# Kernel tuning notes

Hardware: AMD Instinct MI355X
Metric: run time of the kernel (lower is better)

The kernel has to match this reference:

```python
import jax, jax.numpy as jnp
import numpy as np

B_SZ = 1
SEQ = 4096
IN_DIM = 1024
D_MODEL = 512
D_INNER = 1024   # expand(2) * d_model
D_STATE = 16
D_CONV = 4
DT_RANK = 32     # ceil(d_model / 16)
N_LAYERS = 2
N_CLASSES = 2


def setup_inputs() -> dict:
    key = jax.random.key(0)
    ks = jax.random.split(key, 12)
    s = 0.02
    x = jax.random.normal(ks[0], (B_SZ, SEQ, IN_DIM), jnp.float32)
    fc1_w = jax.random.normal(ks[1], (D_MODEL, IN_DIM), jnp.float32) * s
    fc1_b = jnp.zeros((D_MODEL,), jnp.float32)
    ln_w = jnp.ones((N_LAYERS, D_MODEL), jnp.float32)
    ln_b = jnp.zeros((N_LAYERS, D_MODEL), jnp.float32)
    in_proj_w = jax.random.normal(ks[2], (N_LAYERS, 2 * D_INNER, D_MODEL), jnp.float32) * s
    conv_w = jax.random.normal(ks[3], (N_LAYERS, D_INNER, D_CONV), jnp.float32) * 0.1
    conv_b = jnp.zeros((N_LAYERS, D_INNER), jnp.float32)
    x_proj_w = jax.random.normal(ks[4], (N_LAYERS, DT_RANK + 2 * D_STATE, D_INNER), jnp.float32) * s
    dt_proj_w = jax.random.normal(ks[5], (N_LAYERS, D_INNER, DT_RANK), jnp.float32) * s
    # bias so softplus(bias) ~ 0.01 (typical dt init)
    dt_proj_b = jnp.full((N_LAYERS, D_INNER), float(np.log(np.expm1(0.01))), jnp.float32)
    A_log = jnp.broadcast_to(jnp.log(jnp.arange(1, D_STATE + 1, dtype=jnp.float32)),
                             (N_LAYERS, D_INNER, D_STATE)).copy()
    D_skip = jnp.ones((N_LAYERS, D_INNER), jnp.float32)
    norm_w = jnp.ones((D_MODEL,), jnp.float32)
    norm_b = jnp.zeros((D_MODEL,), jnp.float32)
    cls_w = jax.random.normal(ks[6], (N_CLASSES, D_MODEL), jnp.float32) * s
    cls_b = jnp.zeros((N_CLASSES,), jnp.float32)
    return {"x": x, "fc1_w": fc1_w, "fc1_b": fc1_b, "ln_w": ln_w, "ln_b": ln_b,
            "in_proj_w": in_proj_w, "conv_w": conv_w, "conv_b": conv_b,
            "x_proj_w": x_proj_w, "dt_proj_w": dt_proj_w, "dt_proj_b": dt_proj_b,
            "A_log": A_log, "D_skip": D_skip, "norm_w": norm_w, "norm_b": norm_b,
            "cls_w": cls_w, "cls_b": cls_b}


def layernorm(h, w, b, eps=1e-5):
    mu = h.mean(-1, keepdims=True)
    var = ((h - mu) ** 2).mean(-1, keepdims=True)
    return (h - mu) * jax.lax.rsqrt(var + eps) * w + b


def mamba_block(h, in_proj_w, conv_w, conv_b, x_proj_w, dt_proj_w, dt_proj_b, A_log, D_skip):
    # h: [B, L, d_model]
    xz = jnp.einsum('bld,ed->ble', h, in_proj_w)          # [B, L, 2*D_INNER]
    xc, z = jnp.split(xz, 2, axis=-1)                     # each [B, L, D_INNER]
    # causal depthwise conv along L (kernel D_CONV)
    xp = jnp.pad(xc, ((0, 0), (D_CONV - 1, 0), (0, 0)))
    conv = sum(xp[:, k:k + xc.shape[1], :] * conv_w[:, k] for k in range(D_CONV))
    xc = jax.nn.silu(conv + conv_b)
    dbc = jnp.einsum('bld,ed->ble', xc, x_proj_w)         # [B, L, DT_RANK + 2*N]
    dt = jax.nn.softplus(jnp.einsum('blr,dr->bld', dbc[..., :DT_RANK], dt_proj_w) + dt_proj_b)
    Bm = dbc[..., DT_RANK:DT_RANK + D_STATE]              # [B, L, N]
    Cm = dbc[..., DT_RANK + D_STATE:]                     # [B, L, N]
    A = -jnp.exp(A_log)                                   # [D_INNER, N]
    dA = jnp.exp(dt[..., None] * A)                       # [B, L, D_INNER, N]
    dBx = dt[..., None] * Bm[:, :, None, :] * xc[..., None]

    def step(s, ins):
        dA_t, dBx_t, C_t = ins
        s = dA_t * s + dBx_t                              # [B, D_INNER, N]
        y = jnp.einsum('bdn,bn->bd', s, C_t)
        return s, y

    s0 = jnp.zeros((h.shape[0], D_INNER, D_STATE), h.dtype)
    _, ys = jax.lax.scan(step, s0, (dA.transpose(1, 0, 2, 3),
                                    dBx.transpose(1, 0, 2, 3),
                                    Cm.transpose(1, 0, 2)))
    y = ys.transpose(1, 0, 2) + xc * D_skip               # [B, L, D_INNER]
    y = y * jax.nn.silu(z)
    return y


def reference(x, fc1_w, fc1_b, ln_w, ln_b, in_proj_w, conv_w, conv_b,
              x_proj_w, dt_proj_w, dt_proj_b, A_log, D_skip,
              norm_w, norm_b, cls_w, cls_b):
    # out_proj of each Mamba layer folded: out_proj_w stored in in_proj? No -> build here.
    # We use the last N_LAYERS rows trick not needed: out projection is d_inner->d_model,
    # reuse in_proj_w transposed halves would be unfaithful, so derive deterministic weights.
    out_proj_w = jnp.stack([
        jax.random.normal(jax.random.fold_in(jax.random.key(7), i),
                          (D_MODEL, D_INNER), jnp.float32) * 0.02
        for i in range(N_LAYERS)])
    h = jax.nn.gelu(jnp.einsum('bli,di->bld', x, fc1_w) + fc1_b)
    for i in range(N_LAYERS):
        res = h
        hn = layernorm(h, ln_w[i], ln_b[i])
        y = mamba_block(hn, in_proj_w[i], conv_w[i], conv_b[i], x_proj_w[i],
                        dt_proj_w[i], dt_proj_b[i], A_log[i], D_skip[i])
        h = jnp.einsum('ble,de->bld', y, out_proj_w[i]) + res
    h = layernorm(h, norm_w, norm_b)
    hidden = h.mean(axis=1)                               # avg aggregation
    pred = hidden @ cls_w.T + cls_b
    return hidden, pred, h
```

## Files before the change

kernel.cpp:

```cpp
#include <hip/hip_runtime.h>
#include <cstdint>
#include <cstddef>

#define SEQ     4096
#define IN_DIM  1024
#define D_MODEL 512
#define D_INNER 1024
#define D_STATE 16
#define DT_RANK 32

#define CHUNK   32
#define NCHUNK  128
#define NREC    16384

#define LOG2E 1.44269504088896f

static const size_t OFF_H     = 0;
static const size_t OFF_PS    = 2097152;
static const size_t OFF_Z     = 6291456;
static const size_t OFF_XC    = 10485760;
static const size_t OFF_DT    = 14680064;
static const size_t OFF_CARRY = 18874368;
static const size_t OFF_HNB   = 20971520;
static const size_t OFF_WIB   = 21495808;
static const size_t OFF_DBCF  = 22020096;
static const size_t OFF_DBCB  = 22282240;
static const size_t OFF_XPWB  = 22413312;
static const size_t OFF_DPWB  = 22446080;
static const size_t OFF_WOUTB = 22462464;
static const size_t OFF_PART  = 22986752;

typedef __attribute__((ext_vector_type(8))) short bf16x8;
typedef __attribute__((ext_vector_type(4))) float f32x4;

__device__ __forceinline__ uint32_t rotl32(uint32_t v, int r) { return (v << r) | (v >> (32 - r)); }

__device__ __forceinline__ void threefry2x32(uint32_t k0, uint32_t k1, uint32_t x0, uint32_t x1,
                                             uint32_t& o0, uint32_t& o1) {
  uint32_t ks0 = k0, ks1 = k1, ks2 = k0 ^ k1 ^ 0x1BD11BDAu;
  x0 += ks0; x1 += ks1;
  const int rotA[4] = {13, 15, 26, 6};
  const int rotB[4] = {17, 29, 16, 24};
  uint32_t ks[3] = {ks0, ks1, ks2};
#pragma unroll
  for (int r = 0; r < 5; ++r) {
    const int* rr = (r & 1) ? rotB : rotA;
#pragma unroll
    for (int j = 0; j < 4; ++j) { x0 += x1; x1 = rotl32(x1, rr[j]); x1 ^= x0; }
    x0 += ks[(r + 1) % 3];
    x1 += ks[(r + 2) % 3] + (uint32_t)(r + 1);
  }
  o0 = x0; o1 = x1;
}

__device__ __forceinline__ float erfinv32(float x) {
  float w = -log1pf(-x * x);
  float p;
  if (w < 5.0f) {
    w -= 2.5f;
    p = 2.81022636e-08f;
    p = fmaf(p, w, 3.43273939e-07f);
    p = fmaf(p, w, -3.5233877e-06f);
    p = fmaf(p, w, -4.39150654e-06f);
    p = fmaf(p, w, 0.00021858087f);
    p = fmaf(p, w, -0.00125372503f);
    p = fmaf(p, w, -0.00417768164f);
    p = fmaf(p, w, 0.246640727f);
    p = fmaf(p, w, 1.50140941f);
  } else {
    w = sqrtf(w) - 3.0f;
    p = -0.000200214257f;
    p = fmaf(p, w, 0.000100950558f);
    p = fmaf(p, w, 0.00134934322f);
    p = fmaf(p, w, -0.00367342844f);
    p = fmaf(p, w, 0.00573950773f);
    p = fmaf(p, w, -0.0076224613f);
    p = fmaf(p, w, 0.00943887047f);
    p = fmaf(p, w, 1.00167406f);
    p = fmaf(p, w, 2.83297682f);
  }
  return p * x;
}

__device__ __forceinline__ float bits_to_normal(uint32_t b) {
  float f = __uint_as_float((b >> 9) | 0x3f800000u) - 1.0f;
  const float lo = -0.99999994f;
  float u = f * (1.0f - lo) + lo;
  u = fmaxf(lo, u);
  return 1.41421356f * erfinv32(u);
}

__device__ __forceinline__ ushort f2bf(float x) {
  uint32_t u = __float_as_uint(x);
  u = (u + 0x7FFFu + ((u >> 16) & 1u)) >> 16;
  return (ushort)u;
}
__device__ __forceinline__ bf16x8 pack8(float4 a, float4 b) {
  bf16x8 v;
  v[0] = f2bf(a.x); v[1] = f2bf(a.y); v[2] = f2bf(a.z); v[3] = f2bf(a.w);
  v[4] = f2bf(b.x); v[5] = f2bf(b.y); v[6] = f2bf(b.z); v[7] = f2bf(b.w);
  return v;
}

__global__ __launch_bounds__(256) void gen_wout(ushort* __restrict__ w) {
  int gid = blockIdx.x * 256 + threadIdx.x;
  int layer = gid >> 19;
  int j = gid & 0x7FFFF;
  uint32_t k0, k1;
  threefry2x32(0u, 7u, 0u, (uint32_t)layer, k0, k1);
  uint32_t o0, o1;
  threefry2x32(k0, k1, 0u, (uint32_t)j, o0, o1);
  w[(size_t)layer * 524288 + j] = f2bf(bits_to_normal(o0 ^ o1) * 0.02f);
}

__global__ __launch_bounds__(256) void f32_to_bf16(const float* __restrict__ in,
                                                   ushort* __restrict__ out, int n8) {
  int i = blockIdx.x * 256 + threadIdx.x;
  if (i >= n8) return;
  const float4* p = (const float4*)(in + (size_t)i * 8);
  *(bf16x8*)(out + (size_t)i * 8) = pack8(p[0], p[1]);
}

__device__ __forceinline__ float silu_f(float v) { return v / (1.0f + exp2f(-LOG2E * v)); }
__device__ __forceinline__ float gelu_f(float v) {
  float v3 = v * v * v;
  return 0.5f * v * (1.0f + tanhf(0.7978845608028654f * (v + 0.044715f * v3)));
}
__device__ __forceinline__ float softplus_f(float v) {
  return fmaxf(v, 0.0f) + log1pf(exp2f(-LOG2E * fabsf(v)));
}

enum { EPI_NONE = 0, EPI_BIAS_GELU = 1, EPI_INPROJ = 2, EPI_SOFTPLUS = 3, EPI_RESID = 4, EPI_DBC = 5 };

template <int EPI, int NT>
__global__ __launch_bounds__(256) void gemm_bf(
    const ushort* __restrict__ A, int lda,
    const ushort* __restrict__ B, int ldb,
    float* __restrict__ C, int ldc, int K,
    const float* __restrict__ bias, float* __restrict__ out2,
    ushort* __restrict__ outb) {
  constexpr int NB = NT / 64;
  __shared__ ushort As[2][64][40];
  __shared__ ushort Bs[2][NT][40];
  const int m0 = blockIdx.y * 64, n0 = blockIdx.x * NT;
  const int tid = threadIdx.x;
  const int arow = tid >> 2, ach = (tid & 3) * 8;
  const int lane = tid & 63, wid = tid >> 6;
  const int lr = lane & 15, lhi = lane >> 4;
  const ushort* Ap  = A + (size_t)(m0 + arow) * lda + ach;
  const ushort* Bp0 = B + (size_t)(n0 + arow) * ldb + ach;
  const ushort* Bp1 = (NB > 1) ? (B + (size_t)(n0 + 64 + arow) * ldb + ach) : Bp0;

  f32x4 acc[NT / 16] = {};
  uint4 ra, rb0, rb1;

  ra  = *(const uint4*)Ap;
  rb0 = *(const uint4*)Bp0;
  if (NB > 1) rb1 = *(const uint4*)Bp1;
  *(uint4*)&As[0][arow][ach] = ra;
  *(uint4*)&Bs[0][arow][ach] = rb0;
  if (NB > 1) *(uint4*)&Bs[0][64 + arow][ach] = rb1;
  __syncthreads();

  const int nk = K >> 5;
  int cur = 0;
  for (int ki = 0; ki < nk; ++ki) {
    const bool more = (ki + 1 < nk);
    if (more) {
      const int k = (ki + 1) << 5;
      ra  = *(const uint4*)(Ap + k);
      rb0 = *(const uint4*)(Bp0 + k);
      if (NB > 1) rb1 = *(const uint4*)(Bp1 + k);
    }
    bf16x8 af = *(const bf16x8*)&As[cur][wid * 16 + lr][lhi * 8];
#pragma unroll
    for (int t = 0; t < NT / 16; ++t) {
      bf16x8 bv = *(const bf16x8*)&Bs[cur][t * 16 + lr][lhi * 8];
      acc[t] = __builtin_amdgcn_mfma_f32_16x16x32_bf16(af, bv, acc[t], 0, 0, 0);
    }
    if (more) {
      *(uint4*)&As[cur ^ 1][arow][ach] = ra;
      *(uint4*)&Bs[cur ^ 1][arow][ach] = rb0;
      if (NB > 1) *(uint4*)&Bs[cur ^ 1][64 + arow][ach] = rb1;
    }
    __syncthreads();
    cur ^= 1;
  }

#pragma unroll
  for (int t = 0; t < NT / 16; ++t) {
    const int n = n0 + t * 16 + lr;
#pragma unroll
    for (int r = 0; r < 4; ++r) {
      const int m = m0 + wid * 16 + lhi * 4 + r;
      float v = acc[t][r];
      if (EPI == EPI_NONE) {
        C[(size_t)m * ldc + n] = v;
      } else if (EPI == EPI_BIAS_GELU) {
        v += bias[n];
        C[(size_t)m * ldc + n] = gelu_f(v);
      } else if (EPI == EPI_SOFTPLUS) {
        v += bias[n];
        C[(size_t)m * ldc + n] = softplus_f(v);
      } else if (EPI == EPI_RESID) {
        C[(size_t)m * ldc + n] += v;
      } else if (EPI == EPI_INPROJ) {
        if (n < D_INNER) C[(size_t)m * D_INNER + n] = v;
        else             out2[(size_t)m * D_INNER + (n - D_INNER)] = silu_f(v);
      } else if (EPI == EPI_DBC) {
        C[(size_t)m * 64 + n] = v;
        outb[(size_t)m * 64 + n] = f2bf(v);
      }
    }
  }
}

template <int BF>
__global__ __launch_bounds__(256) void ln_rows(const float* __restrict__ in,
                                               const float* __restrict__ w,
                                               const float* __restrict__ b,
                                               float* __restrict__ outf,
                                               ushort* __restrict__ outb) {
  __shared__ double red[4];
  const int row = blockIdx.x, t = threadIdx.x;
  const float* r = in + (size_t)row * D_MODEL;
  double x0 = (double)r[t], x1 = (double)r[t + 256];
  double s = x0 + x1;
#pragma unroll
  for (int o = 32; o >= 1; o >>= 1) s += __shfl_down(s, o);
  int wid = t >> 6, lane = t & 63;
  if (lane == 0) red[wid] = s;
  __syncthreads();
  double mu = (red[0] + red[1] + red[2] + red[3]) * (1.0 / 512.0);
  __syncthreads();
  double d0 = x0 - mu, d1 = x1 - mu;
  double v = d0 * d0 + d1 * d1;
#pragma unroll
  for (int o = 32; o >= 1; o >>= 1) v += __shfl_down(v, o);
  if (lane == 0) red[wid] = v;
  __syncthreads();
  double var = (red[0] + red[1] + red[2] + red[3]) * (1.0 / 512.0);
  double rs = rsqrt(var + 1e-5);
  float o0 = (float)(d0 * rs * (double)w[t] + (double)b[t]);
  float o1 = (float)(d1 * rs * (double)w[t + 256] + (double)b[t + 256]);
  if (BF) {
    outb[(size_t)row * D_MODEL + t]       = f2bf(o0);
    outb[(size_t)row * D_MODEL + t + 256] = f2bf(o1);
  } else {
    outf[(size_t)row * D_MODEL + t]       = o0;
    outf[(size_t)row * D_MODEL + t + 256] = o1;
  }
}

__global__ __launch_bounds__(256) void conv_silu2(const float* __restrict__ xcr,
                                                  const float* __restrict__ cw,
                                                  const float* __restrict__ cb,
                                                  float* __restrict__ outf,
                                                  ushort* __restrict__ outb) {
  const int l = blockIdx.x;
  for (int q = 0; q < 4; ++q) {
    const int d = threadIdx.x + q * 256;
    float acc = cb[d];
#pragma unroll
    for (int k = 0; k < 4; ++k) {
      const int ll = l + k - 3;
      const float xv = (ll >= 0) ? xcr[(size_t)ll * D_INNER + d] : 0.0f;
      acc = fmaf(xv, cw[d * 4 + k], acc);
    }
    float o = silu_f(acc);
    outf[(size_t)l * D_INNER + d] = o;
    outb[(size_t)l * D_INNER + d] = f2bf(o);
  }
}

__global__ __launch_bounds__(256) void scanA(const float* __restrict__ dt,
                                             const float* __restrict__ dbc,
                                             const float* __restrict__ xc,
                                             const float* __restrict__ Alog,
                                             float* __restrict__ P, float* __restrict__ S) {
  const int c = blockIdx.y;
  const int d = blockIdx.x * 256 + threadIdx.x;
  float a2[16], s[16];
#pragma unroll
  for (int q = 0; q < 4; ++q) {
    float4 al = *(const float4*)(Alog + (size_t)d * 16 + q * 4);
    a2[4*q+0] = -expf(al.x) * LOG2E; a2[4*q+1] = -expf(al.y) * LOG2E;
    a2[4*q+2] = -expf(al.z) * LOG2E; a2[4*q+3] = -expf(al.w) * LOG2E;
  }
#pragma unroll
  for (int n = 0; n < 16; ++n) s[n] = 0.0f;
  float sdt = 0.0f;
  const int l0 = c * CHUNK;
#pragma unroll 2
  for (int t = 0; t < CHUNK; ++t) {
    const int l = l0 + t;
    const float dtv = dt[(size_t)l * D_INNER + d];
    const float xv  = xc[(size_t)l * D_INNER + d];
    const float dx = dtv * xv;
    sdt += dtv;
    float bv[16];
    const float4* B4 = (const float4*)(dbc + (size_t)l * 64 + DT_RANK);
    *(float4*)&bv[0]  = B4[0]; *(float4*)&bv[4]  = B4[1];
    *(float4*)&bv[8]  = B4[2]; *(float4*)&bv[12] = B4[3];
#pragma unroll
    for (int n = 0; n < 16; ++n)
      s[n] = fmaf(exp2f(dtv * a2[n]), s[n], bv[n] * dx);
  }
  float4* Sp = (float4*)(S + (size_t)c * NREC + (size_t)d * 16);
  float4* Pp = (float4*)(P + (size_t)c * NREC + (size_t)d * 16);
#pragma unroll
  for (int q = 0; q < 4; ++q) {
    Sp[q] = make_float4(s[4*q], s[4*q+1], s[4*q+2], s[4*q+3]);
    Pp[q] = make_float4(exp2f(a2[4*q]*sdt), exp2f(a2[4*q+1]*sdt),
                        exp2f(a2[4*q+2]*sdt), exp2f(a2[4*q+3]*sdt));
  }
}

__global__ __launch_bounds__(256) void scanB(const float* __restrict__ P,
                                             const float* __restrict__ S,
                                             float* __restrict__ carry) {
  int idx = blockIdx.x * 256 + threadIdx.x;
  float cr = 0.0f;
  for (int c = 0; c < NCHUNK; ++c) {
    size_t k = (size_t)c * NREC + idx;
    carry[k] = cr;
    cr = fmaf(P[k], cr, S[k]);
  }
}

__global__ __launch_bounds__(256) void scanC(const float* __restrict__ dt,
                                             const float* __restrict__ dbc,
                                             const float* __restrict__ xc,
                                             const float* __restrict__ Alog,
                                             const float* __restrict__ carry,
                                             const float* __restrict__ Dskip,
                                             const float* __restrict__ zs,
                                             ushort* __restrict__ yb) {
  const int c = blockIdx.y;
  const int d = blockIdx.x * 256 + threadIdx.x;
  float a2[16], s[16];
#pragma unroll
  for (int q = 0; q < 4; ++q) {
    float4 al = *(const float4*)(Alog + (size_t)d * 16 + q * 4);
    a2[4*q+0] = -expf(al.x) * LOG2E; a2[4*q+1] = -expf(al.y) * LOG2E;
    a2[4*q+2] = -expf(al.z) * LOG2E; a2[4*q+3] = -expf(al.w) * LOG2E;
    float4 cr = *(const float4*)(carry + (size_t)c * NREC + (size_t)d * 16 + q * 4);
    s[4*q+0] = cr.x; s[4*q+1] = cr.y; s[4*q+2] = cr.z; s[4*q+3] = cr.w;
  }
  const float dsk = Dskip[d];
  const int l0 = c * CHUNK;
#pragma unroll 2
  for (int t = 0; t < CHUNK; ++t) {
    const int l = l0 + t;
    const float dtv = dt[(size_t)l * D_INNER + d];
    const float xv  = xc[(size_t)l * D_INNER + d];
    const float dx = dtv * xv;
    float bv[16], cv[16];
    const float4* B4 = (const float4*)(dbc + (size_t)l * 64 + DT_RANK);
    *(float4*)&bv[0]  = B4[0]; *(float4*)&bv[4]  = B4[1];
    *(float4*)&bv[8]  = B4[2]; *(float4*)&bv[12] = B4[3];
    *(float4*)&cv[0]  = B4[4]; *(float4*)&cv[4]  = B4[5];
    *(float4*)&cv[8]  = B4[6]; *(float4*)&cv[12] = B4[7];
    float acc = 0.0f;
#pragma unroll
    for (int n = 0; n < 16; ++n) {
      s[n] = fmaf(exp2f(dtv * a2[n]), s[n], bv[n] * dx);
      acc = fmaf(s[n], cv[n], acc);
    }
    float yv = fmaf(xv, dsk, acc);
    yb[(size_t)l * D_INNER + d] = f2bf(yv * zs[(size_t)l * D_INNER + d]);
  }
}

__global__ __launch_bounds__(512) void colsum(const float* __restrict__ h, double* __restrict__ part) {
  int d = threadIdx.x;
  int r0 = blockIdx.x * 128;
  double s = 0.0;
  for (int r = 0; r < 128; ++r) s += (double)h[(size_t)(r0 + r) * D_MODEL + d];
  part[blockIdx.x * D_MODEL + d] = s;
}

__global__ __launch_bounds__(512) void head_k(const double* __restrict__ part,
                                              const float* __restrict__ cls_w,
                                              const float* __restrict__ cls_b,
                                              float* __restrict__ out) {
  __shared__ double l0[512], l1[512];
  int d = threadIdx.x;
  double s = 0.0;
  for (int b = 0; b < 32; ++b) s += part[b * D_MODEL + d];
  double hv = s * (1.0 / 4096.0);
  out[d] = (float)hv;
  l0[d] = hv * (double)cls_w[d];
  l1[d] = hv * (double)cls_w[D_MODEL + d];
  __syncthreads();
  for (int o = 256; o > 0; o >>= 1) {
    if (d < o) { l0[d] += l0[d + o]; l1[d] += l1[d + o]; }
    __syncthreads();
  }
  if (d == 0) { out[512] = (float)(l0[0] + (double)cls_b[0]); out[513] = (float)(l1[0] + (double)cls_b[1]); }
}

extern "C" void kernel_launch(void* const* d_in, const int* in_sizes, int n_in,
                              void* d_out, int out_size, void* d_ws, size_t ws_size,
                              hipStream_t stream) {
  const float* x         = (const float*)d_in[0];
  const float* fc1_w     = (const float*)d_in[1];
  const float* fc1_b     = (const float*)d_in[2];
  const float* ln_w      = (const float*)d_in[3];
  const float* ln_b      = (const float*)d_in[4];
  const float* in_proj_w = (const float*)d_in[5];
  const float* conv_w    = (const float*)d_in[6];
  const float* conv_b    = (const float*)d_in[7];
  const float* x_proj_w  = (const float*)d_in[8];
  const float* dt_proj_w = (const float*)d_in[9];
  const float* dt_proj_b = (const float*)d_in[10];
  const float* A_log     = (const float*)d_in[11];
  const float* D_skip    = (const float*)d_in[12];
  const float* norm_w    = (const float*)d_in[13];
  const float* norm_b    = (const float*)d_in[14];
  const float* cls_w     = (const float*)d_in[15];
  const float* cls_b     = (const float*)d_in[16];
  float* out = (float*)d_out;
  float* ws  = (float*)d_ws;

  float*  h_buf   = ws + OFF_H;
  float*  xcraw   = ws + OFF_PS;
  float*  P_buf   = ws + OFF_PS;
  float*  S_buf   = ws + OFF_PS + 2097152;
  ushort* y_bf    = (ushort*)(ws + OFF_PS);
  float*  z_buf   = ws + OFF_Z;
  float*  xc_buf  = ws + OFF_XC;
  float*  dt_buf  = ws + OFF_DT;
  ushort* x_bf    = (ushort*)(ws + OFF_DT);
  ushort* xc_bf   = (ushort*)(ws + OFF_DT);
  float*  carry_b = ws + OFF_CARRY;
  ushort* fc1w_bf = (ushort*)(ws + OFF_CARRY);
  ushort* hn_bf   = (ushort*)(ws + OFF_HNB);
  ushort* Wi_bf   = (ushort*)(ws + OFF_WIB);
  float*  dbc_f   = ws + OFF_DBCF;
  ushort* dbc_bf  = (ushort*)(ws + OFF_DBCB);
  ushort* xpw_bf  = (ushort*)(ws + OFF_XPWB);
  ushort* dpw_bf  = (ushort*)(ws + OFF_DPWB);
  ushort* wout_bf = (ushort*)(ws + OFF_WOUTB);
  double* part    = (double*)(ws + OFF_PART);

  gen_wout<<<4096, 256, 0, stream>>>(wout_bf);

  f32_to_bf16<<<2048, 256, 0, stream>>>(x, x_bf, 524288);
  f32_to_bf16<<<256, 256, 0, stream>>>(fc1_w, fc1w_bf, 65536);

  gemm_bf<EPI_BIAS_GELU, 128><<<dim3(4, 64), 256, 0, stream>>>(
      x_bf, IN_DIM, fc1w_bf, IN_DIM, h_buf, D_MODEL, IN_DIM, fc1_b, nullptr, nullptr);

  for (int i = 0; i < 2; ++i) {
    ln_rows<1><<<4096, 256, 0, stream>>>(h_buf, ln_w + i * D_MODEL, ln_b + i * D_MODEL,
                                         nullptr, hn_bf);
    f32_to_bf16<<<512, 256, 0, stream>>>(in_proj_w + (size_t)i * 2 * D_INNER * D_MODEL,
                                         Wi_bf, 131072);
    gemm_bf<EPI_INPROJ, 128><<<dim3(16, 64), 256, 0, stream>>>(
        hn_bf, D_MODEL, Wi_bf, D_MODEL, xcraw, D_INNER, D_MODEL, nullptr, z_buf, nullptr);
    conv_silu2<<<4096, 256, 0, stream>>>(xcraw, conv_w + (size_t)i * D_INNER * 4,
                                         conv_b + i * D_INNER, xc_buf, xc_bf);
    f32_to_bf16<<<32, 256, 0, stream>>>(x_proj_w + (size_t)i * 64 * D_INNER, xpw_bf, 8192);
    f32_to_bf16<<<16, 256, 0, stream>>>(dt_proj_w + (size_t)i * D_INNER * DT_RANK, dpw_bf, 4096);
    gemm_bf<EPI_DBC, 64><<<dim3(1, 64), 256, 0, stream>>>(
        xc_bf, D_INNER, xpw_bf, D_INNER, dbc_f, 64, D_INNER, nullptr, nullptr, dbc_bf);
    gemm_bf<EPI_SOFTPLUS, 128><<<dim3(8, 64), 256, 0, stream>>>(
        dbc_bf, 64, dpw_bf, DT_RANK, dt_buf, D_INNER, DT_RANK,
        dt_proj_b + i * D_INNER, nullptr, nullptr);
    const float* Alog_i = A_log + (size_t)i * D_INNER * D_STATE;
    scanA<<<dim3(4, NCHUNK), 256, 0, stream>>>(dt_buf, dbc_f, xc_buf, Alog_i, P_buf, S_buf);
    scanB<<<64, 256, 0, stream>>>(P_buf, S_buf, carry_b);
    scanC<<<dim3(4, NCHUNK), 256, 0, stream>>>(dt_buf, dbc_f, xc_buf, Alog_i, carry_b,
                                               D_skip + i * D_INNER, z_buf, y_bf);
    gemm_bf<EPI_RESID, 128><<<dim3(4, 64), 256, 0, stream>>>(
        y_bf, D_INNER, wout_bf + (size_t)i * 524288, D_INNER, h_buf, D_MODEL, D_INNER,
        nullptr, nullptr, nullptr);
  }

  ln_rows<0><<<4096, 256, 0, stream>>>(h_buf, norm_w, norm_b, out + 514, nullptr);
  colsum<<<32, 512, 0, stream>>>(out + 514, part);
  head_k<<<1, 512, 0, stream>>>(part, cls_w, cls_b, out);
}
```

Before: 400.1 us.

## Batch all fp32-to-bf16 weight conversions into one launch and add 128x128 in_proj GEMM

Result: faster. 384.7 us (-3.8%).

```diff
diff --git a/kernel.cpp b/kernel.cpp
--- a/kernel.cpp
+++ b/kernel.cpp
@@ -22,13 +22,14 @@
 static const size_t OFF_DT    = 14680064;
 static const size_t OFF_CARRY = 18874368;
 static const size_t OFF_HNB   = 20971520;
-static const size_t OFF_WIB   = 21495808;
-static const size_t OFF_DBCF  = 22020096;
-static const size_t OFF_DBCB  = 22282240;
-static const size_t OFF_XPWB  = 22413312;
-static const size_t OFF_DPWB  = 22446080;
-static const size_t OFF_WOUTB = 22462464;
-static const size_t OFF_PART  = 22986752;
+static const size_t OFF_FC1WB = 22020096;
+static const size_t OFF_WIB   = 22282240;
+static const size_t OFF_XPWB  = 23330816;
+static const size_t OFF_DPWB  = 23396352;
+static const size_t OFF_DBCF  = 23429120;
+static const size_t OFF_DBCB  = 23691264;
+static const size_t OFF_WOUTB = 23822336;
+static const size_t OFF_PART  = 24346624;
 
 typedef __attribute__((ext_vector_type(8))) short bf16x8;
 typedef __attribute__((ext_vector_type(4))) float f32x4;
@@ -113,12 +114,22 @@
   w[(size_t)layer * 524288 + j] = f2bf(bits_to_normal(o0 ^ o1) * 0.02f);
 }
 
-__global__ __launch_bounds__(256) void f32_to_bf16(const float* __restrict__ in,
-                                                   ushort* __restrict__ out, int n8) {
-  int i = blockIdx.x * 256 + threadIdx.x;
-  if (i >= n8) return;
-  const float4* p = (const float4*)(in + (size_t)i * 8);
-  *(bf16x8*)(out + (size_t)i * 8) = pack8(p[0], p[1]);
+__global__ __launch_bounds__(256) void convert_all(
+    const float* __restrict__ x,   const float* __restrict__ fc1w,
+    const float* __restrict__ ipw, const float* __restrict__ xpw,
+    const float* __restrict__ dpw,
+    ushort* __restrict__ xb, ushort* __restrict__ fc1wb, ushort* __restrict__ ipwb,
+    ushort* __restrict__ xpwb, ushort* __restrict__ dpwb) {
+  int gid = blockIdx.x * 256 + threadIdx.x;
+  const float* src; ushort* dst; size_t off;
+  if (gid < 524288)      { src = x;    dst = xb;    off = gid; }
+  else if (gid < 589824) { src = fc1w; dst = fc1wb; off = gid - 524288; }
+  else if (gid < 851968) { src = ipw;  dst = ipwb;  off = gid - 589824; }
+  else if (gid < 868352) { src = xpw;  dst = xpwb;  off = gid - 851968; }
+  else if (gid < 876544) { src = dpw;  dst = dpwb;  off = gid - 868352; }
+  else return;
+  const float4* p = (const float4*)(src + off * 8);
+  *(bf16x8*)(dst + off * 8) = pack8(p[0], p[1]);
 }
 
 __device__ __forceinline__ float silu_f(float v) { return v / (1.0f + exp2f(-LOG2E * v)); }
@@ -210,6 +221,78 @@
       } else if (EPI == EPI_DBC) {
         C[(size_t)m * 64 + n] = v;
         outb[(size_t)m * 64 + n] = f2bf(v);
+      }
+    }
+  }
+}
+
+template <int EPI>
+__global__ __launch_bounds__(256) void gemm_bf128(
+    const ushort* __restrict__ A, int lda,
+    const ushort* __restrict__ B, int ldb,
+    float* __restrict__ C, int ldc, int K,
+    const float* __restrict__ bias, float* __restrict__ out2) {
+  __shared__ ushort As[2][128][40];
+  __shared__ ushort Bs[2][128][40];
+  const int m0 = blockIdx.y * 128, n0 = blockIdx.x * 128;
+  const int tid = threadIdx.x;
+  const int lane = tid & 63, wid = tid >> 6;
+  const int lr = lane & 15, lhi = lane >> 4;
+  const int r0_ = tid >> 2, ach = (tid & 3) * 8;
+  const ushort* Ap0 = A + (size_t)(m0 + r0_) * lda + ach;
+  const ushort* Ap1 = A + (size_t)(m0 + r0_ + 64) * lda + ach;
+  const ushort* Bp0 = B + (size_t)(n0 + r0_) * ldb + ach;
+  const ushort* Bp1 = B + (size_t)(n0 + r0_ + 64) * ldb + ach;
+
+  f32x4 acc[16] = {};
+  uint4 ra0, ra1, rb0, rb1;
+
+  ra0 = *(const uint4*)Ap0; ra1 = *(const uint4*)Ap1;
+  rb0 = *(const uint4*)Bp0; rb1 = *(const uint4*)Bp1;
+  *(uint4*)&As[0][r0_][ach] = ra0; *(uint4*)&As[0][r0_ + 64][ach] = ra1;
+  *(uint4*)&Bs[0][r0_][ach] = rb0; *(uint4*)&Bs[0][r0_ + 64][ach] = rb1;
+  __syncthreads();
+
+  const int nk = K >> 5;
+  int cur = 0;
+  for (int ki = 0; ki < nk; ++ki) {
+    const bool more = (ki + 1 < nk);
+    if (more) {
+      const int k = (ki + 1) << 5;
+      ra0 = *(const uint4*)(Ap0 + k); ra1 = *(const uint4*)(Ap1 + k);
+      rb0 = *(const uint4*)(Bp0 + k); rb1 = *(const uint4*)(Bp1 + k);
+    }
+    bf16x8 af0 = *(const bf16x8*)&As[cur][wid * 32 + lr][lhi * 8];
+    bf16x8 af1 = *(const bf16x8*)&As[cur][wid * 32 + 16 + lr][lhi * 8];
+#pragma unroll
+    for (int t = 0; t < 8; ++t) {
+      bf16x8 bv = *(const bf16x8*)&Bs[cur][t * 16 + lr][lhi * 8];
+      acc[t]     = __builtin_amdgcn_mfma_f32_16x16x32_bf16(af0, bv, acc[t], 0, 0, 0);
+      acc[8 + t] = __builtin_amdgcn_mfma_f32_16x16x32_bf16(af1, bv, acc[8 + t], 0, 0, 0);
+    }
+    if (more) {
+      *(uint4*)&As[cur ^ 1][r0_][ach] = ra0; *(uint4*)&As[cur ^ 1][r0_ + 64][ach] = ra1;
+      *(uint4*)&Bs[cur ^ 1][r0_][ach] = rb0; *(uint4*)&Bs[cur ^ 1][r0_ + 64][ach] = rb1;
+    }
+    __syncthreads();
+    cur ^= 1;
+  }
+
+#pragma unroll
+  for (int fr = 0; fr < 2; ++fr) {
+#pragma unroll
+    for (int t = 0; t < 8; ++t) {
+      const int n = n0 + t * 16 + lr;
+#pragma unroll
+      for (int r = 0; r < 4; ++r) {
+        const int m = m0 + wid * 32 + fr * 16 + lhi * 4 + r;
+        float v = acc[fr * 8 + t][r];
+        if (EPI == EPI_INPROJ) {
+          if (n < D_INNER) C[(size_t)m * D_INNER + n] = v;
+          else             out2[(size_t)m * D_INNER + (n - D_INNER)] = silu_f(v);
+        } else {
+          C[(size_t)m * ldc + n] = v;
+        }
       }
     }
   }
@@ -434,20 +517,19 @@
   ushort* x_bf    = (ushort*)(ws + OFF_DT);
   ushort* xc_bf   = (ushort*)(ws + OFF_DT);
   float*  carry_b = ws + OFF_CARRY;
-  ushort* fc1w_bf = (ushort*)(ws + OFF_CARRY);
   ushort* hn_bf   = (ushort*)(ws + OFF_HNB);
+  ushort* fc1w_bf = (ushort*)(ws + OFF_FC1WB);
   ushort* Wi_bf   = (ushort*)(ws + OFF_WIB);
+  ushort* xpw_bf  = (ushort*)(ws + OFF_XPWB);
+  ushort* dpw_bf  = (ushort*)(ws + OFF_DPWB);
   float*  dbc_f   = ws + OFF_DBCF;
   ushort* dbc_bf  = (ushort*)(ws + OFF_DBCB);
-  ushort* xpw_bf  = (ushort*)(ws + OFF_XPWB);
-  ushort* dpw_bf  = (ushort*)(ws + OFF_DPWB);
   ushort* wout_bf = (ushort*)(ws + OFF_WOUTB);
   double* part    = (double*)(ws + OFF_PART);
 
   gen_wout<<<4096, 256, 0, stream>>>(wout_bf);
-
-  f32_to_bf16<<<2048, 256, 0, stream>>>(x, x_bf, 524288);
-  f32_to_bf16<<<256, 256, 0, stream>>>(fc1_w, fc1w_bf, 65536);
+  convert_all<<<3424, 256, 0, stream>>>(x, fc1_w, in_proj_w, x_proj_w, dt_proj_w,
+                                        x_bf, fc1w_bf, Wi_bf, xpw_bf, dpw_bf);
 
   gemm_bf<EPI_BIAS_GELU, 128><<<dim3(4, 64), 256, 0, stream>>>(
       x_bf, IN_DIM, fc1w_bf, IN_DIM, h_buf, D_MODEL, IN_DIM, fc1_b, nullptr, nullptr);
@@ -455,18 +537,16 @@
   for (int i = 0; i < 2; ++i) {
     ln_rows<1><<<4096, 256, 0, stream>>>(h_buf, ln_w + i * D_MODEL, ln_b + i * D_MODEL,
                                          nullptr, hn_bf);
-    f32_to_bf16<<<512, 256, 0, stream>>>(in_proj_w + (size_t)i * 2 * D_INNER * D_MODEL,
-                                         Wi_bf, 131072);
-    gemm_bf<EPI_INPROJ, 128><<<dim3(16, 64), 256, 0, stream>>>(
-        hn_bf, D_MODEL, Wi_bf, D_MODEL, xcraw, D_INNER, D_MODEL, nullptr, z_buf, nullptr);
+    gemm_bf128<EPI_INPROJ><<<dim3(16, 32), 256, 0, stream>>>(
+        hn_bf, D_MODEL, Wi_bf + (size_t)i * 1048576, D_MODEL, xcraw, D_INNER, D_MODEL,
+        nullptr, z_buf);
     conv_silu2<<<4096, 256, 0, stream>>>(xcraw, conv_w + (size_t)i * D_INNER * 4,
                                          conv_b + i * D_INNER, xc_buf, xc_bf);
-    f32_to_bf16<<<32, 256, 0, stream>>>(x_proj_w + (size_t)i * 64 * D_INNER, xpw_bf, 8192);
-    f32_to_bf16<<<16, 256, 0, stream>>>(dt_proj_w + (size_t)i * D_INNER * DT_RANK, dpw_bf, 4096);
     gemm_bf<EPI_DBC, 64><<<dim3(1, 64), 256, 0, stream>>>(
-        xc_bf, D_INNER, xpw_bf, D_INNER, dbc_f, 64, D_INNER, nullptr, nullptr, dbc_bf);
+        xc_bf, D_INNER, xpw_bf + (size_t)i * 65536, D_INNER, dbc_f, 64, D_INNER,
+        nullptr, nullptr, dbc_bf);
     gemm_bf<EPI_SOFTPLUS, 128><<<dim3(8, 64), 256, 0, stream>>>(
-        dbc_bf, 64, dpw_bf, DT_RANK, dt_buf, D_INNER, DT_RANK,
+        dbc_bf, 64, dpw_bf + (size_t)i * 32768, DT_RANK, dt_buf, D_INNER, DT_RANK,
         dt_proj_b + i * D_INNER, nullptr, nullptr);
     const float* Alog_i = A_log + (size_t)i * D_INNER * D_STATE;
     scanA<<<dim3(4, NCHUNK), 256, 0, stream>>>(dt_buf, dbc_f, xc_buf, Alog_i, P_buf, S_buf);
```
